# Performance work log

Measured on AMD Instinct MI355X. Metric: run time of the kernel, lower is better.

## Reference

```python
import jax, jax.numpy as jnp
import numpy as np

MU = 0.99
THRESHOLD = 1.0

def setup_inputs() -> dict:
    key = jax.random.key(0)
    k1, k2, k3 = jax.random.split(key, 3)
    N, W, T, K = 16, 512, 1024, 2048
    x = jax.random.normal(k1, (N, W, T), jnp.float32)
    k = jax.random.normal(k2, (K, W), jnp.float32) * 0.02
    k_sum = jax.random.normal(k3, (K, W), jnp.float32) * 0.02
    k_elem = jnp.ones((K,), jnp.float32)
    return {"x": x, "k": k, "k_sum": k_sum, "k_elem": k_elem}

def reference(x, k, k_sum, k_elem):
    N, W, T = x.shape
    K = k.shape[0]
    # preprocess: [N, W, T] -> [N*T, W]
    xf = x.transpose(0, 2, 1).reshape(-1, W)
    prenorm = jnp.linalg.norm(xf - jnp.mean(xf)) / np.sqrt(xf.size)
    # quantise: pairwise squared distances [N*T, K] then argmin
    dist = (jnp.sum(xf * xf, axis=-1, keepdims=True)
            - 2.0 * (xf @ k.T)
            + jnp.sum(k * k, axis=-1)[None, :])
    min_dist = jnp.min(dist, axis=-1)
    x_l = jnp.argmin(dist, axis=-1)
    fit = jnp.mean(min_dist)
    # dequantise: embedding gather
    x_d = k[x_l]
    # update_k: scatter-sum cluster stats + EMA + conditional reset (no grad)
    _k_sum = jax.ops.segment_sum(xf, x_l, num_segments=K)
    _k_elem = jax.ops.segment_sum(jnp.ones((xf.shape[0],), xf.dtype), x_l, num_segments=K)
    k_rand = jax.random.permutation(jax.random.key(42), xf)[:K]  # N*T >= K so no tiling
    k_sum_new = MU * k_sum + (1.0 - MU) * _k_sum
    k_elem_new = MU * k_elem + (1.0 - MU) * _k_elem
    usage = (k_elem_new[:, None] >= THRESHOLD).astype(xf.dtype)
    k_new = usage * (k_sum_new / k_elem_new[:, None]) + (1.0 - usage) * k_rand
    k_prob = _k_elem / jnp.sum(_k_elem)
    entropy = -jnp.sum(k_prob * jnp.log(k_prob + 1e-8))
    dk = jnp.linalg.norm(k_new - k) / np.sqrt(K * W)
    # commit loss + straight-through estimator
    commit_loss = jnp.sum((jax.lax.stop_gradient(x_d) - xf) ** 2) / xf.size
    x_d = xf + jax.lax.stop_gradient(x_d - xf)
    # postprocess
    x_d = x_d.reshape(N, T, W).transpose(0, 2, 1)
    x_l = x_l.reshape(N, T)
    return (x_l, x_d, commit_loss, fit, prenorm, entropy, dk, k_new, k_sum_new, k_elem_new)
```

## Files before the change

### kernel.cpp

```cpp
#include <hip/hip_runtime.h>
#include <stdint.h>


#define W_   512
#define T_   1024
#define K_   2048
#define NT_  16384

#define RNG_VARIANT 0
#define XG_CAP 1536

typedef unsigned short ushort_t;
typedef __attribute__((ext_vector_type(8))) short short8;
typedef __attribute__((ext_vector_type(4))) float f32x4;

#define OFF_XHI     0u
#define OFF_XLO     16777216u
#define OFF_KHI     33554432u
#define OFF_KLO     35651584u
#define OFF_PM1     37748736u
#define OFF_PM2     39845888u
#define OFF_XG      37748736u
#define R_HIST      39845888u
#define R_CUR       39878656u
#define R_BASE      39911424u
#define R_SLOT      39944448u
#define OFF_PACKED  40894464u
#define OFF_FLIST   41025536u
#define OFF_X2      41091072u
#define OFF_K2      41156608u
#define OFF_SCAL    41164800u
#define OFF_COUNTS  41165056u
#define OFF_CURSOR  41173248u
#define OFF_RANK1   41181440u
#define OFF_RANK2   41246976u
#define ZERO_LEN    147712u
#define OFF_BITS1   41312512u
#define OFF_BITS2   41378048u
#define OFF_OFFS    41443584u
#define OFF_ROWL    41452032u
#define OFF_KRAND   41517568u

#define O_XL    0u
#define O_XD    16384u
#define O_SC    8404992u
#define O_KNEW  8404997u
#define O_KSN   9453573u
#define O_KEN   10502149u

__device__ __forceinline__ float bf2f(ushort_t u) {
  return __uint_as_float(((unsigned)u) << 16);
}
__device__ __forceinline__ ushort_t f2bf(float v) {
  unsigned u = __float_as_uint(v);
  unsigned r = u + 0x7FFFu + ((u >> 16) & 1u);
  return (ushort_t)(r >> 16);
}
__device__ __forceinline__ void gload_lds16(const void* g, void* l) {
  __builtin_amdgcn_global_load_lds(
      (const __attribute__((address_space(1))) unsigned*)g,
      (__attribute__((address_space(3))) unsigned*)l, 16, 0, 0);
}

__device__ __forceinline__ void tf2x32(uint32_t k0, uint32_t k1,
                                       uint32_t x0, uint32_t x1,
                                       uint32_t& o0, uint32_t& o1) {
  const uint32_t ks2 = k0 ^ k1 ^ 0x1BD11BDAu;
  x0 += k0; x1 += k1;
#define ROUND4(a,b,c,d) \
  x0+=x1; x1=(x1<<(a))|(x1>>(32-(a))); x1^=x0; \
  x0+=x1; x1=(x1<<(b))|(x1>>(32-(b))); x1^=x0; \
  x0+=x1; x1=(x1<<(c))|(x1>>(32-(c))); x1^=x0; \
  x0+=x1; x1=(x1<<(d))|(x1>>(32-(d))); x1^=x0;
  ROUND4(13,15,26,6)  x0+=k1;  x1+=ks2+1u;
  ROUND4(17,29,16,24) x0+=ks2; x1+=k0+2u;
  ROUND4(13,15,26,6)  x0+=k0;  x1+=k1+3u;
  ROUND4(17,29,16,24) x0+=k1;  x1+=ks2+4u;
  ROUND4(13,15,26,6)  x0+=ks2; x1+=k0+5u;
#undef ROUND4
  o0 = x0; o1 = x1;
}

__global__ void vq_prep_x(const float* __restrict__ x, ushort_t* __restrict__ xhi,
                          ushort_t* __restrict__ xlo, float* __restrict__ x2,
                          float* __restrict__ scal) {
  __shared__ float tile[64][65];
  __shared__ float x2s[64];
  __shared__ float rs[4], rq[4];
  int b = blockIdx.x;
  int n = b >> 4, tc = b & 15;
  int t0 = tc * 64;
  int tid = threadIdx.x;
  if (tid < 64) x2s[tid] = 0.f;
  __syncthreads();
  float gs = 0.f, gq = 0.f;
  const size_t xb = (size_t)n * (W_ * T_);
  int tl = tid & 63, wg = tid >> 6;
  int wl = 2 * (tid & 31), tg = tid >> 5;
  for (int p = 0; p < 8; p++) {
    int w0 = p * 64;
#pragma unroll 4
    for (int s = 0; s < 16; s++) {
      int w = s * 4 + wg;
      tile[tl][w] = x[xb + (size_t)(w0 + w) * T_ + t0 + tl];
    }
    __syncthreads();
#pragma unroll
    for (int s = 0; s < 8; s++) {
      int t = s * 8 + tg;
      float v0 = tile[t][wl], v1 = tile[t][wl + 1];
      ushort_t h0 = f2bf(v0); ushort_t l0 = f2bf(v0 - bf2f(h0));
      ushort_t h1 = f2bf(v1); ushort_t l1 = f2bf(v1 - bf2f(h1));
      size_t row = (size_t)n * 1024 + t0 + t;
      ushort2 hv; hv.x = h0; hv.y = h1;
      ushort2 lv; lv.x = l0; lv.y = l1;
      *(ushort2*)&xhi[row * 512 + w0 + wl] = hv;
      *(ushort2*)&xlo[row * 512 + w0 + wl] = lv;
      gs += v0 + v1;
      float part = v0 * v0 + v1 * v1;
      gq += part;
      for (int off = 16; off; off >>= 1) part += __shfl_down(part, off, 32);
      if ((tid & 31) == 0) x2s[t] += part;
    }
    __syncthreads();
  }
  for (int off = 32; off; off >>= 1) { gs += __shfl_down(gs, off, 64); gq += __shfl_down(gq, off, 64); }
  if ((tid & 63) == 0) { rs[tid >> 6] = gs; rq[tid >> 6] = gq; }
  __syncthreads();
  if (tid == 0) {
    atomicAdd(&scal[0], rs[0] + rs[1] + rs[2] + rs[3]);
    atomicAdd(&scal[1], rq[0] + rq[1] + rq[2] + rq[3]);
  }
  if (tid < 64) x2[n * 1024 + t0 + tid] = x2s[tid];
}

__global__ void vq_prep_k(const float* __restrict__ k, ushort_t* __restrict__ khi,
                          ushort_t* __restrict__ klo, float* __restrict__ k2v) {
  int tid = threadIdx.x;
  int row = blockIdx.x * 8 + (tid >> 5);
  int wl = tid & 31;
  const float* kr = k + (size_t)row * 512;
  float acc = 0.f;
#pragma unroll
  for (int c = 0; c < 4; c++) {
    int w = c * 128 + wl * 4;
    float4 v = *(const float4*)(kr + w);
    ushort4 hv, lv;
    hv.x = f2bf(v.x); lv.x = f2bf(v.x - bf2f(hv.x));
    hv.y = f2bf(v.y); lv.y = f2bf(v.y - bf2f(hv.y));
    hv.z = f2bf(v.z); lv.z = f2bf(v.z - bf2f(hv.z));
    hv.w = f2bf(v.w); lv.w = f2bf(v.w - bf2f(hv.w));
    *(ushort4*)&khi[(size_t)row * 512 + w] = hv;
    *(ushort4*)&klo[(size_t)row * 512 + w] = lv;
    acc += v.x * v.x + v.y * v.y + v.z * v.z + v.w * v.w;
  }
  for (int off = 16; off; off >>= 1) acc += __shfl_down(acc, off, 32);
  if (wl == 0) k2v[row] = acc;
}

__global__ void vq_bits(uint32_t* __restrict__ bits1, uint32_t* __restrict__ bits2) {
  uint32_t i = blockIdx.x * 256 + threadIdx.x;
  uint32_t o0, o1;
#if RNG_VARIANT == 2
  uint32_t a0, a1, b0, b1, c0, c1, d0, d1;
  tf2x32(0u, 42u, 0u, 2u, a0, a1);
  tf2x32(0u, 42u, 1u, 3u, b0, b1);
  uint32_t keyA0 = a0, keyA1 = b0, s1k0 = a1, s1k1 = b1;
  tf2x32(keyA0, keyA1, 0u, 2u, c0, c1);
  tf2x32(keyA0, keyA1, 1u, 3u, d0, d1);
  uint32_t s2k0 = c1, s2k1 = d1;
  uint32_t lo = (i < 8192u) ? i : (i - 8192u);
  tf2x32(s1k0, s1k1, lo, lo + 8192u, o0, o1);
  bits1[i] = (i < 8192u) ? o0 : o1;
  tf2x32(s2k0, s2k1, lo, lo + 8192u, o0, o1);
  bits2[i] = (i < 8192u) ? o0 : o1;
#else
  uint32_t a0, a1, b0, b1, c0, c1, d0, d1;
  tf2x32(0u, 42u, 0u, 0u, a0, a1);
  tf2x32(0u, 42u, 0u, 1u, b0, b1);
  tf2x32(a0, a1, 0u, 0u, c0, c1);
  tf2x32(a0, a1, 0u, 1u, d0, d1);
  (void)c0; (void)c1;
  tf2x32(b0, b1, 0u, i, o0, o1);
#if RNG_VARIANT == 0
  bits1[i] = o1;
#else
  bits1[i] = o0;
#endif
  tf2x32(d0, d1, 0u, i, o0, o1);
#if RNG_VARIANT == 0
  bits2[i] = o1;
#else
  bits2[i] = o0;
#endif
#endif
}

__global__ void vq_hist(const uint32_t* __restrict__ bits1, const uint32_t* __restrict__ bits2,
                        int* __restrict__ hist) {
  int i = blockIdx.x * 256 + threadIdx.x;
  atomicAdd(&hist[bits1[i] >> 20], 1);
  atomicAdd(&hist[4096 + (bits2[i] >> 20)], 1);
}

__global__ void vq_hscan(const int* __restrict__ hist, int* __restrict__ base) {
  int s = blockIdx.x;
  int t = threadIdx.x;
  __shared__ int wsum[4];
  int p = 0;
  int loc[16];
#pragma unroll
  for (int c = 0; c < 16; c++) { loc[c] = hist[s * 4096 + t * 16 + c]; p += loc[c]; }
  int orig = p;
  int lane = t & 63, wave = t >> 6;
#pragma unroll
  for (int off = 1; off < 64; off <<= 1) {
    int v = __shfl_up(p, off, 64);
    if (lane >= off) p += v;
  }
  if (lane == 63) wsum[wave] = p;
  __syncthreads();
  int add = 0;
  for (int w = 0; w < 4; w++) if (w < wave) add += wsum[w];
  int excl = p + add - orig;
#pragma unroll
  for (int c = 0; c < 16; c++) {
    base[s * 4100 + t * 16 + c] = excl;
    excl += loc[c];
  }
  if (t == 255) base[s * 4100 + 4096] = excl;
}

__global__ void vq_scatter(const uint32_t* __restrict__ bits1, const uint32_t* __restrict__ bits2,
                           const int* __restrict__ base, int* __restrict__ cur,
                           int* __restrict__ slot) {
  int i = blockIdx.x * 256 + threadIdx.x;
  {
    int b = bits1[i] >> 20;
    int pos = atomicAdd(&cur[b], 1);
    slot[base[b] + pos] = i;
  }
  {
    int b = bits2[i] >> 20;
    int pos = atomicAdd(&cur[4096 + b], 1);
    slot[16384 + base[4100 + b] + pos] = i;
  }
}

__global__ void vq_rank2(const uint32_t* __restrict__ bits1, const uint32_t* __restrict__ bits2,
                         const int* __restrict__ base, const int* __restrict__ slot,
                         uint32_t* __restrict__ rank1, uint32_t* __restrict__ rank2) {
  int g = blockIdx.x * 256 + threadIdx.x;
  int s = g >> 14, i = g & 16383;
  const uint32_t* bits = s ? bits2 : bits1;
  uint32_t ki = bits[i];
  int b = ki >> 20;
  int lo = base[s * 4100 + b], hi = base[s * 4100 + b + 1];
  int cnt = lo;
  for (int e = lo; e < hi; e++) {
    int j = slot[s * 16384 + e];
    uint32_t kj = bits[j];
    cnt += (kj < ki) || (kj == ki && j < i);
  }
  if (s) rank2[i] = (uint32_t)cnt; else rank1[i] = (uint32_t)cnt;
}

__global__ void vq_krand(const uint32_t* __restrict__ rank1, const uint32_t* __restrict__ rank2,
                         int* __restrict__ krand) {
  int i = blockIdx.x * 256 + threadIdx.x;
  uint32_t j = rank1[i] & 16383u;
  uint32_t p = rank2[j];
  if (p < K_) krand[p] = i;
}

__global__ __launch_bounds__(256, 2) void vq_argmin_mfma(
    const ushort_t* __restrict__ xhi, const ushort_t* __restrict__ xlo,
    const ushort_t* __restrict__ khi, const ushort_t* __restrict__ klo,
    const float* __restrict__ x2, const float* __restrict__ k2,
    unsigned long long* __restrict__ pm1, float* __restrict__ pm2) {
  __shared__ __align__(16) char smem[65536];
  int tid = threadIdx.x;
  int bx = blockIdx.x & 127, by = blockIdx.x >> 7;
  int row0 = bx * 128, col0 = by * 128;
  int lane = tid & 63, wid = tid >> 6;
  int wm = wid >> 1, wn = wid & 1;
  int lr = lane & 15, quad = lane >> 4;

  const char* gb[4];
  gb[0] = (const char*)xhi + (size_t)row0 * 1024;
  gb[1] = (const char*)xlo + (size_t)row0 * 1024;
  gb[2] = (const char*)khi + (size_t)col0 * 1024;
  gb[3] = (const char*)klo + (size_t)col0 * 1024;
  uint32_t goff[4], loff[4];
#pragma unroll
  for (int it = 0; it < 4; it++) {
    int cid = it * 256 + tid;
    int row = cid >> 3;
    int cc = (cid & 7) ^ (row & 7);
    goff[it] = row * 1024 + cc * 16;
    loff[it] = cid * 16;
  }
  uint32_t aoff[4], boff[4];
#pragma unroll
  for (int i = 0; i < 4; i++) {
    int ra = wm * 64 + i * 16 + lr;
    aoff[i] = ra * 128 + ((quad ^ (ra & 7)) * 16);
    int rb = wn * 64 + i * 16 + lr;
    boff[i] = rb * 128 + ((quad ^ (rb & 7)) * 16);
  }
  f32x4 acc[4][4] = {};

  for (int kt = 0; kt < 8; kt++) {
    uint32_t kofs = (uint32_t)kt * 128;
#pragma unroll
    for (int tl = 0; tl < 4; tl++)
#pragma unroll
      for (int it = 0; it < 4; it++)
        gload_lds16(gb[tl] + goff[it] + kofs, &smem[tl * 16384 + loff[it]]);
    __syncthreads();
#pragma unroll
    for (int kk = 0; kk < 2; kk++) {
      uint32_t kx = (uint32_t)kk << 6;
      short8 ah[4], al[4], bh[4], bl[4];
#pragma unroll
      for (int i = 0; i < 4; i++) {
        ah[i] = *(const short8*)&smem[(aoff[i] ^ kx)];
        al[i] = *(const short8*)&smem[16384 + (aoff[i] ^ kx)];
        bh[i] = *(const short8*)&smem[32768 + (boff[i] ^ kx)];
        bl[i] = *(const short8*)&smem[49152 + (boff[i] ^ kx)];
      }
#pragma unroll
      for (int i = 0; i < 4; i++)
#pragma unroll
        for (int j = 0; j < 4; j++) {
          acc[i][j] = __builtin_amdgcn_mfma_f32_16x16x32_bf16(ah[i], bh[j], acc[i][j], 0, 0, 0);
          acc[i][j] = __builtin_amdgcn_mfma_f32_16x16x32_bf16(ah[i], bl[j], acc[i][j], 0, 0, 0);
          acc[i][j] = __builtin_amdgcn_mfma_f32_16x16x32_bf16(al[i], bh[j], acc[i][j], 0, 0, 0);
        }
    }
    __syncthreads();
  }

  unsigned long long* L1 = (unsigned long long*)smem;
  float* L2f = (float*)&smem[32768];
  float k2c[4];
#pragma unroll
  for (int j = 0; j < 4; j++) k2c[j] = k2[col0 + wn * 64 + j * 16 + lr];
#pragma unroll
  for (int i = 0; i < 4; i++) {
#pragma unroll
    for (int r = 0; r < 4; r++) {
      int row_l = wm * 64 + i * 16 + quad * 4 + r;
      float x2r = x2[row0 + row_l];
      float m1 = 3.4e38f, m2 = 3.4e38f; int mi = 0;
#pragma unroll
      for (int j = 0; j < 4; j++) {
        float d = (x2r - 2.0f * acc[i][j][r]) + k2c[j];
        int kg = col0 + wn * 64 + j * 16 + lr;
        if (d < m1) { m2 = m1; m1 = d; mi = kg; } else m2 = fminf(m2, d);
      }
      L1[row_l * 32 + wn * 16 + lr] =
          (((unsigned long long)__float_as_uint(m1)) << 32) | (unsigned)mi;
      L2f[row_l * 32 + wn * 16 + lr] = m2;
    }
  }
  __syncthreads();
  if (tid < 128) {
    unsigned long long b1 = L1[tid * 32];
    float b2 = L2f[tid * 32];
    for (int c = 1; c < 32; c++) {
      unsigned long long v = L1[tid * 32 + c];
      float vf = L2f[tid * 32 + c];
      if (v < b1) { b2 = fminf(b2, __uint_as_float((unsigned)(b1 >> 32))); b1 = v; }
      else b2 = fminf(b2, __uint_as_float((unsigned)(v >> 32)));
      b2 = fminf(b2, vf);
    }
    pm1[(size_t)by * NT_ + row0 + tid] = b1;
    pm2[(size_t)by * NT_ + row0 + tid] = b2;
  }
}

__global__ void vq_merge(const unsigned long long* __restrict__ pm1,
                         const float* __restrict__ pm2,
                         unsigned long long* __restrict__ packed,
                         int* __restrict__ flist, int* __restrict__ nflag) {
  int r = blockIdx.x * 256 + threadIdx.x;
  unsigned long long b1 = pm1[r];
  float b2 = pm2[r];
  for (int c = 1; c < 16; c++) {
    unsigned long long v = pm1[(size_t)c * NT_ + r];
    float vf = pm2[(size_t)c * NT_ + r];
    if (v < b1) { b2 = fminf(b2, __uint_as_float((unsigned)(b1 >> 32))); b1 = v; }
    else b2 = fminf(b2, __uint_as_float((unsigned)(v >> 32)));
    b2 = fminf(b2, vf);
  }
  if ((b2 - __uint_as_float((unsigned)(b1 >> 32))) < 3e-4f) {
    packed[r] = 0xFFFFFFFFFFFFFFFFull;
    int pos = atomicAdd(nflag, 1);
    flist[pos] = r;
  } else {
    packed[r] = b1;
  }
}

__global__ void vq_gatherx(const float* __restrict__ x, const int* __restrict__ flist,
                           const int* __restrict__ nflag, float* __restrict__ xg) {
  int nf = *nflag; if (nf > XG_CAP) nf = XG_CAP;
  int total = nf * 512;
  for (int e = blockIdx.x * 256 + threadIdx.x; e < total; e += gridDim.x * 256) {
    int ii = e >> 9, c = e & 511;
    int r = flist[ii];
    xg[e] = x[(size_t)(r >> 10) * 524288 + (size_t)c * 1024 + (r & 1023)];
  }
}

__global__ void vq_repair(const float* __restrict__ x, const float* __restrict__ k,
                          const float* __restrict__ xg,
                          const float* __restrict__ x2, const float* __restrict__ k2,
                          const int* __restrict__ flist, const int* __restrict__ nflag,
                          unsigned long long* __restrict__ packed) {
  __shared__ float xs[8][512];
  __shared__ unsigned long long part[8][4];
  int tid = threadIdx.x;
  int lane = tid & 63, wave = tid >> 6;
  int nf = *nflag;
  int ngrp = (nf + 7) >> 3;
  int nwork = ngrp * 8;
  for (int wi = blockIdx.x; wi < nwork; wi += gridDim.x) {
    int g = wi >> 3, c = wi & 7;
    int base = g * 8;
    for (int e = tid; e < 8 * 512; e += 256) {
      int rr = e >> 9, cc = e & 511;
      int ii = base + rr;
      float v = 0.f;
      if (ii < nf) {
        if (ii < XG_CAP) v = xg[ii * 512 + cc];
        else { int r = flist[ii]; v = x[(size_t)(r >> 10) * 524288 + (size_t)cc * 1024 + (r & 1023)]; }
      }
      xs[rr][cc] = v;
    }
    __syncthreads();
    int j = c * 256 + tid;
    const float4* kr = (const float4*)(k + (size_t)j * 512);
    float dot[8] = {0.f, 0.f, 0.f, 0.f, 0.f, 0.f, 0.f, 0.f};
    for (int w4 = 0; w4 < 128; w4++) {
      float4 kv = kr[w4];
#pragma unroll
      for (int rr = 0; rr < 8; rr++) {
        const float4 xv = *(const float4*)&xs[rr][w4 * 4];
        dot[rr] = fmaf(xv.x, kv.x, dot[rr]);
        dot[rr] = fmaf(xv.y, kv.y, dot[rr]);
        dot[rr] = fmaf(xv.z, kv.z, dot[rr]);
        dot[rr] = fmaf(xv.w, kv.w, dot[rr]);
      }
    }
    float k2j = k2[j];
#pragma unroll
    for (int rr = 0; rr < 8; rr++) {
      int ii = base + rr;
      unsigned long long pv = 0xFFFFFFFFFFFFFFFFull;
      if (ii < nf) {
        int r = flist[ii];
        float d = (x2[r] - 2.0f * dot[rr]) + k2j;
        pv = (((unsigned long long)__float_as_uint(d)) << 32) | (unsigned)j;
      }
      for (int off = 32; off; off >>= 1) {
        unsigned long long o = __shfl_down(pv, off, 64);
        if (o < pv) pv = o;
      }
      if (lane == 0) part[rr][wave] = pv;
    }
    __syncthreads();
    if (tid < 8) {
      int ii = base + tid;
      if (ii < nf) {
        unsigned long long m = part[tid][0];
        if (part[tid][1] < m) m = part[tid][1];
        if (part[tid][2] < m) m = part[tid][2];
        if (part[tid][3] < m) m = part[tid][3];
        atomicMin(&packed[flist[ii]], m);
      }
    }
    __syncthreads();
  }
}

__global__ void vq_cnt2(const unsigned long long* __restrict__ packed,
                        float* __restrict__ counts, float* __restrict__ scal,
                        float* __restrict__ out) {
  int tid = threadIdx.x;
  int r = blockIdx.x * 256 + tid;
  unsigned long long p = packed[r];
  unsigned idx = (unsigned)(p & 0xFFFFFFFFull);
  float md = __uint_as_float((unsigned)(p >> 32));
  out[O_XL + r] = (float)idx;
  atomicAdd(&counts[idx], 1.0f);
  float s = md;
  for (int off = 32; off; off >>= 1) s += __shfl_down(s, off, 64);
  __shared__ float rs[4];
  if ((tid & 63) == 0) rs[tid >> 6] = s;
  __syncthreads();
  if (tid == 0) atomicAdd(&scal[2], rs[0] + rs[1] + rs[2] + rs[3]);
}

__global__ void vq_scan(const float* __restrict__ counts, int* __restrict__ offs) {
  __shared__ int ls[256];
  int t = threadIdx.x;
  int s = 0;
#pragma unroll
  for (int c = 0; c < 8; c++) s += (int)counts[t * 8 + c];
  ls[t] = s;
  __syncthreads();
  if (t == 0) {
    int run = 0;
    for (int i = 0; i < 256; i++) { int v = ls[i]; ls[i] = run; run += v; }
  }
  __syncthreads();
  int base = ls[t];
#pragma unroll
  for (int c = 0; c < 8; c++) {
    offs[t * 8 + c] = base;
    base += (int)counts[t * 8 + c];
  }
  if (t == 255) offs[2048] = base;
}

__global__ void vq_fill(const unsigned long long* __restrict__ packed,
                        const int* __restrict__ offs, int* __restrict__ cursor,
                        int* __restrict__ rowl) {
  int r = blockIdx.x * 256 + threadIdx.x;
  int idx = (int)(packed[r] & 0xFFFFFFFFull);
  int pos = atomicAdd(&cursor[idx], 1);
  rowl[offs[idx] + pos] = r;
}

__global__ void vq_xd(const float* __restrict__ k,
                      const unsigned long long* __restrict__ packed,
                      float* __restrict__ out) {
  __shared__ float kb[16][513];
  __shared__ int lrow[16];
  int rb = blockIdx.x;
  int row0 = rb * 16;
  int n = row0 >> 10, t0 = row0 & 1023;
  int tid = threadIdx.x;
  if (tid < 16) lrow[tid] = (int)(packed[row0 + tid] & 0xFFFFFFFFull);
  __syncthreads();
  for (int i = tid; i < 16 * 512; i += 256) {
    int rr = i >> 9, c = i & 511;
    kb[rr][c] = k[(size_t)lrow[rr] * 512 + c];
  }
  __syncthreads();
  int tp = tid & 15, wp = tid >> 4;
  float* xd = out + O_XD;
  int t = t0 + tp;
#pragma unroll 4
  for (int wi = 0; wi < 32; wi++) {
    int w = wi * 16 + wp;
    xd[(size_t)n * 524288 + (size_t)w * 1024 + t] = kb[tp][w];
  }
}

__global__ void vq_knew_csr(const ushort_t* __restrict__ xhi, const ushort_t* __restrict__ xlo,
                            const float* __restrict__ k, const float* __restrict__ ksum_in,
                            const float* __restrict__ kelem_in, const int* __restrict__ offs,
                            const int* __restrict__ rowl, const int* __restrict__ krand,
                            float* __restrict__ out, float* __restrict__ scal) {
  int j = blockIdx.x, tid = threadIdx.x;
  int o0 = offs[j], o1 = offs[j + 1];
  float s0 = 0.f, s1 = 0.f;
  for (int p = o0; p < o1; p++) {
    int r = rowl[p];
    const ushort_t* hp = &xhi[(size_t)r * 512];
    const ushort_t* lp = &xlo[(size_t)r * 512];
    s0 += bf2f(hp[tid]) + bf2f(lp[tid]);
    s1 += bf2f(hp[tid + 256]) + bf2f(lp[tid + 256]);
  }
  float cnt = (float)(o1 - o0);
  float ken = 0.99f * kelem_in[j] + 0.01f * cnt;
  bool use = (ken >= 1.0f);
  int ir = krand[j] & 16383;
  float dd = 0.f;
  {
    float ksn = 0.99f * ksum_in[(size_t)j * 512 + tid] + 0.01f * s0;
    out[O_KSN + (size_t)j * 512 + tid] = ksn;
    float kn = use ? (ksn / ken)
                   : (bf2f(xhi[(size_t)ir * 512 + tid]) + bf2f(xlo[(size_t)ir * 512 + tid]));
    out[O_KNEW + (size_t)j * 512 + tid] = kn;
    float d = kn - k[(size_t)j * 512 + tid];
    dd += d * d;
  }
  {
    int w = tid + 256;
    float ksn = 0.99f * ksum_in[(size_t)j * 512 + w] + 0.01f * s1;
    out[O_KSN + (size_t)j * 512 + w] = ksn;
    float kn = use ? (ksn / ken)
                   : (bf2f(xhi[(size_t)ir * 512 + w]) + bf2f(xlo[(size_t)ir * 512 + w]));
    out[O_KNEW + (size_t)j * 512 + w] = kn;
    float d = kn - k[(size_t)j * 512 + w];
    dd += d * d;
  }
  for (int off = 32; off; off >>= 1) dd += __shfl_down(dd, off, 64);
  __shared__ float r4[4];
  if ((tid & 63) == 0) r4[tid >> 6] = dd;
  __syncthreads();
  if (tid == 0) {
    atomicAdd(&scal[3], r4[0] + r4[1] + r4[2] + r4[3]);
    out[O_KEN + j] = ken;
  }
}

__global__ void vq_fin(const float* __restrict__ counts, const float* __restrict__ scal,
                       float* __restrict__ out) {
  int tid = threadIdx.x;
  float e = 0.f;
  for (int j = tid; j < K_; j += 256) {
    float p = counts[j] * (1.0f / 16384.0f);
    e -= p * logf(p + 1e-8f);
  }
  for (int off = 32; off; off >>= 1) e += __shfl_down(e, off, 64);
  __shared__ float r[4];
  if ((tid & 63) == 0) r[tid >> 6] = e;
  __syncthreads();
  if (tid == 0) {
    float ent = r[0] + r[1] + r[2] + r[3];
    float sum = scal[0], sumsq = scal[1], fits = scal[2], d2 = scal[3];
    const float S = 8388608.f;
    out[O_SC + 0] = fits / S;
    out[O_SC + 1] = fits / 16384.f;
    out[O_SC + 2] = sqrtf((sumsq - sum * sum / S) / S);
    out[O_SC + 3] = ent;
    out[O_SC + 4] = sqrtf(d2 / 1048576.f);
  }
}

extern "C" void kernel_launch(void* const* d_in, const int* in_sizes, int n_in,
                              void* d_out, int out_size, void* d_ws, size_t ws_size,
                              hipStream_t stream) {
  (void)in_sizes; (void)n_in; (void)out_size; (void)ws_size;
  const float* x        = (const float*)d_in[0];
  const float* k        = (const float*)d_in[1];
  const float* ksum_in  = (const float*)d_in[2];
  const float* kelem_in = (const float*)d_in[3];
  float* out = (float*)d_out;
  uint8_t* ws = (uint8_t*)d_ws;

  ushort_t* xhi = (ushort_t*)(ws + OFF_XHI);
  ushort_t* xlo = (ushort_t*)(ws + OFF_XLO);
  ushort_t* khi = (ushort_t*)(ws + OFF_KHI);
  ushort_t* klo = (ushort_t*)(ws + OFF_KLO);
  unsigned long long* pm1 = (unsigned long long*)(ws + OFF_PM1);
  float*    pm2    = (float*)(ws + OFF_PM2);
  float*    xg     = (float*)(ws + OFF_XG);
  int*      rhist  = (int*)(ws + R_HIST);
  int*      rcur   = (int*)(ws + R_CUR);
  int*      rbase  = (int*)(ws + R_BASE);
  int*      rslot  = (int*)(ws + R_SLOT);
  unsigned long long* packed = (unsigned long long*)(ws + OFF_PACKED);
  int*      flist  = (int*)(ws + OFF_FLIST);
  float*    x2v    = (float*)(ws + OFF_X2);
  float*    k2v    = (float*)(ws + OFF_K2);
  float*    scal   = (float*)(ws + OFF_SCAL);
  int*      nflag  = (int*)(ws + OFF_SCAL + 32);
  float*    counts = (float*)(ws + OFF_COUNTS);
  int*      cursor = (int*)(ws + OFF_CURSOR);
  uint32_t* rank1  = (uint32_t*)(ws + OFF_RANK1);
  uint32_t* rank2  = (uint32_t*)(ws + OFF_RANK2);
  uint32_t* bits1  = (uint32_t*)(ws + OFF_BITS1);
  uint32_t* bits2  = (uint32_t*)(ws + OFF_BITS2);
  int*      offs   = (int*)(ws + OFF_OFFS);
  int*      rowl   = (int*)(ws + OFF_ROWL);
  int*      krand  = (int*)(ws + OFF_KRAND);

  hipMemsetAsync(ws + OFF_SCAL, 0, ZERO_LEN, stream);
  hipMemsetAsync(ws + R_HIST, 0, 65536, stream);

  vq_prep_x<<<256, 256, 0, stream>>>(x, xhi, xlo, x2v, scal);
  vq_prep_k<<<256, 256, 0, stream>>>(k, khi, klo, k2v);
  vq_bits<<<64, 256, 0, stream>>>(bits1, bits2);
  vq_hist<<<64, 256, 0, stream>>>(bits1, bits2, rhist);
  vq_hscan<<<2, 256, 0, stream>>>(rhist, rbase);
  vq_scatter<<<64, 256, 0, stream>>>(bits1, bits2, rbase, rcur, rslot);
  vq_rank2<<<128, 256, 0, stream>>>(bits1, bits2, rbase, rslot, rank1, rank2);
  vq_krand<<<64, 256, 0, stream>>>(rank1, rank2, krand);
  vq_argmin_mfma<<<2048, 256, 0, stream>>>(xhi, xlo, khi, klo, x2v, k2v, pm1, pm2);
  vq_merge<<<64, 256, 0, stream>>>(pm1, pm2, packed, flist, nflag);
  vq_gatherx<<<256, 256, 0, stream>>>(x, flist, nflag, xg);
  vq_repair<<<512, 256, 0, stream>>>(x, k, xg, x2v, k2v, flist, nflag, packed);
  vq_cnt2<<<64, 256, 0, stream>>>(packed, counts, scal, out);
  vq_scan<<<1, 256, 0, stream>>>(counts, offs);
  vq_fill<<<64, 256, 0, stream>>>(packed, offs, cursor, rowl);
  vq_xd<<<1024, 256, 0, stream>>>(k, packed, out);
  vq_knew_csr<<<2048, 256, 0, stream>>>(xhi, xlo, k, ksum_in, kelem_in, offs, rowl, krand, out, scal);
  vq_fin<<<1, 256, 0, stream>>>(counts, scal, out);
}
```

Before: 356.8 us.

## Fuse RNG histogram into bits kernel and use fragment-ordered LDS layout in argmin GEMM

The random-bits kernel now builds the histogram directly with atomics, which removes the separate vq_hist launch and its reload of the bits arrays. In the MFMA argmin kernel, the global-to-LDS copy is remapped so each wave's MFMA fragments sit contiguously in shared memory. Every lane then reads a linear 16-byte chunk, which replaces the XOR-swizzled addressing and its per-load address arithmetic and is meant to avoid bank conflicts. The risk is that the global load pattern becomes less coalesced, since each group of four 16-byte chunks is now scattered across rows.

```diff
diff --git a/kernel.cpp b/kernel.cpp
--- a/kernel.cpp
+++ b/kernel.cpp
@@ -158,9 +158,11 @@
   if (wl == 0) k2v[row] = acc;
 }
 
-__global__ void vq_bits(uint32_t* __restrict__ bits1, uint32_t* __restrict__ bits2) {
+__global__ void vq_bits(uint32_t* __restrict__ bits1, uint32_t* __restrict__ bits2,
+                        int* __restrict__ hist) {
   uint32_t i = blockIdx.x * 256 + threadIdx.x;
   uint32_t o0, o1;
+  uint32_t v1, v2;
 #if RNG_VARIANT == 2
   uint32_t a0, a1, b0, b1, c0, c1, d0, d1;
   tf2x32(0u, 42u, 0u, 2u, a0, a1);
@@ -171,9 +173,9 @@
   uint32_t s2k0 = c1, s2k1 = d1;
   uint32_t lo = (i < 8192u) ? i : (i - 8192u);
   tf2x32(s1k0, s1k1, lo, lo + 8192u, o0, o1);
-  bits1[i] = (i < 8192u) ? o0 : o1;
+  v1 = (i < 8192u) ? o0 : o1;
   tf2x32(s2k0, s2k1, lo, lo + 8192u, o0, o1);
-  bits2[i] = (i < 8192u) ? o0 : o1;
+  v2 = (i < 8192u) ? o0 : o1;
 #else
   uint32_t a0, a1, b0, b1, c0, c1, d0, d1;
   tf2x32(0u, 42u, 0u, 0u, a0, a1);
@@ -183,24 +185,21 @@
   (void)c0; (void)c1;
   tf2x32(b0, b1, 0u, i, o0, o1);
 #if RNG_VARIANT == 0
-  bits1[i] = o1;
+  v1 = o1;
 #else
-  bits1[i] = o0;
+  v1 = o0;
 #endif
   tf2x32(d0, d1, 0u, i, o0, o1);
 #if RNG_VARIANT == 0
-  bits2[i] = o1;
+  v2 = o1;
 #else
-  bits2[i] = o0;
+  v2 = o0;
 #endif
 #endif
-}
-
-__global__ void vq_hist(const uint32_t* __restrict__ bits1, const uint32_t* __restrict__ bits2,
-                        int* __restrict__ hist) {
-  int i = blockIdx.x * 256 + threadIdx.x;
-  atomicAdd(&hist[bits1[i] >> 20], 1);
-  atomicAdd(&hist[4096 + (bits2[i] >> 20)], 1);
+  bits1[i] = v1;
+  bits2[i] = v2;
+  atomicAdd(&hist[v1 >> 20], 1);
+  atomicAdd(&hist[4096 + (v2 >> 20)], 1);
 }
 
 __global__ void vq_hscan(const int* __restrict__ hist, int* __restrict__ base) {
@@ -295,19 +294,17 @@
 #pragma unroll
   for (int it = 0; it < 4; it++) {
     int cid = it * 256 + tid;
-    int row = cid >> 3;
-    int cc = (cid & 7) ^ (row & 7);
-    goff[it] = row * 1024 + cc * 16;
-    loff[it] = cid * 16;
-  }
-  uint32_t aoff[4], boff[4];
-#pragma unroll
-  for (int i = 0; i < 4; i++) {
-    int ra = wm * 64 + i * 16 + lr;
-    aoff[i] = ra * 128 + ((quad ^ (ra & 7)) * 16);
-    int rb = wn * 64 + i * 16 + lr;
-    boff[i] = rb * 128 + ((quad ^ (rb & 7)) * 16);
-  }
+    int lr5 = cid & 15;
+    int quad5 = (cid >> 4) & 3;
+    int kk5 = (cid >> 6) & 1;
+    int i5 = (cid >> 7) & 3;
+    int g25 = (cid >> 9) & 1;
+    int grow = g25 * 64 + i5 * 16 + lr5;
+    goff[it] = (uint32_t)(grow * 1024 + kk5 * 64 + quad5 * 16);
+    loff[it] = (uint32_t)(cid * 16);
+  }
+  const int abase = wm * 8192 + lane * 16;
+  const int bbase = wn * 8192 + lane * 16;
   f32x4 acc[4][4] = {};
 
   for (int kt = 0; kt < 8; kt++) {
@@ -320,14 +317,15 @@
     __syncthreads();
 #pragma unroll
     for (int kk = 0; kk < 2; kk++) {
-      uint32_t kx = (uint32_t)kk << 6;
       short8 ah[4], al[4], bh[4], bl[4];
 #pragma unroll
       for (int i = 0; i < 4; i++) {
-        ah[i] = *(const short8*)&smem[(aoff[i] ^ kx)];
-        al[i] = *(const short8*)&smem[16384 + (aoff[i] ^ kx)];
-        bh[i] = *(const short8*)&smem[32768 + (boff[i] ^ kx)];
-        bl[i] = *(const short8*)&smem[49152 + (boff[i] ^ kx)];
+        int ao = abase + (i * 2 + kk) * 1024;
+        int bo = bbase + (i * 2 + kk) * 1024;
+        ah[i] = *(const short8*)&smem[ao];
+        al[i] = *(const short8*)&smem[16384 + ao];
+        bh[i] = *(const short8*)&smem[32768 + bo];
+        bl[i] = *(const short8*)&smem[49152 + bo];
       }
 #pragma unroll
       for (int i = 0; i < 4; i++)
@@ -676,8 +674,7 @@
 
   vq_prep_x<<<256, 256, 0, stream>>>(x, xhi, xlo, x2v, scal);
   vq_prep_k<<<256, 256, 0, stream>>>(k, khi, klo, k2v);
-  vq_bits<<<64, 256, 0, stream>>>(bits1, bits2);
-  vq_hist<<<64, 256, 0, stream>>>(bits1, bits2, rhist);
+  vq_bits<<<64, 256, 0, stream>>>(bits1, bits2, rhist);
   vq_hscan<<<2, 256, 0, stream>>>(rhist, rbase);
   vq_scatter<<<64, 256, 0, stream>>>(bits1, bits2, rbase, rcur, rslot);
   vq_rank2<<<128, 256, 0, stream>>>(bits1, bits2, rbase, rslot, rank1, rank2);
```

Result: slower. 410.1 us (+15.0%).
